# Kernel optimization log

Measured on AMD Instinct MI355X. Metric: run time of the kernel, lower is better.

The kernel has to match this reference:

```python
import jax, jax.numpy as jnp
import numpy as np

NUM_BUOYS = 16384
TIME_STEPS = 8
FEATURE_DIM = 64
ID_EMB_DIM = 1024  # must equal gru_hidden_size for steps 4/5 to type-check
HIDDEN = 1024
NUM_EMB = 100
INPUT_SIZE = FEATURE_DIM + ID_EMB_DIM


def setup_inputs() -> dict:
    key = jax.random.key(0)
    k = jax.random.split(key, 7)
    s = 1.0 / np.sqrt(HIDDEN)
    return {
        "buoy_obs": jax.random.normal(k[0], (NUM_BUOYS, TIME_STEPS, FEATURE_DIM), jnp.float32),
        "buoy_ids": jax.random.randint(k[1], (NUM_BUOYS,), 0, NUM_EMB),
        "emb": jax.random.normal(k[2], (NUM_EMB, ID_EMB_DIM), jnp.float32),
        "W_ih": jax.random.uniform(k[3], (3 * HIDDEN, INPUT_SIZE), jnp.float32, -s, s),
        "W_hh": jax.random.uniform(k[4], (3 * HIDDEN, HIDDEN), jnp.float32, -s, s),
        "b_ih": jax.random.uniform(k[5], (3 * HIDDEN,), jnp.float32, -s, s),
        "b_hh": jax.random.uniform(k[6], (3 * HIDDEN,), jnp.float32, -s, s),
    }


def _gru_cell(x, h, W_ih, W_hh, b_ih, b_hh):
    # PyTorch GRU gate layout: [r, z, n]
    gi = x @ W_ih.T + b_ih  # (N, 3H)
    gh = h @ W_hh.T + b_hh  # (N, 3H)
    gi_r, gi_z, gi_n = jnp.split(gi, 3, axis=-1)
    gh_r, gh_z, gh_n = jnp.split(gh, 3, axis=-1)
    r = jax.nn.sigmoid(gi_r + gh_r)
    z = jax.nn.sigmoid(gi_z + gh_z)
    n = jnp.tanh(gi_n + r * gh_n)
    return (1.0 - z) * n + z * h


def reference(buoy_obs, buoy_ids, emb, W_ih, W_hh, b_ih, b_hh):
    num_buoys = buoy_obs.shape[0]
    id_emb = emb[buoy_ids]  # (N, E)
    h = jnp.zeros((num_buoys, HIDDEN), buoy_obs.dtype)
    outs = []
    # three unrolled steps: input = [obs_t, id_emb]
    for t in range(3):
        x = jnp.concatenate([buoy_obs[:, t, :], id_emb], axis=-1)
        h = _gru_cell(x, h, W_ih, W_hh, b_ih, b_hh)
        outs.append(h)
    # step 4: input = [out0, obs_1]
    x = jnp.concatenate([outs[0], buoy_obs[:, 1, :]], axis=-1)
    h = _gru_cell(x, h, W_ih, W_hh, b_ih, b_hh)
    second_out = h
    # step 5: input = [out4, obs_2]
    x = jnp.concatenate([second_out, buoy_obs[:, 2, :]], axis=-1)
    h = _gru_cell(x, h, W_ih, W_hh, b_ih, b_hh)
    # AdaptiveMaxPool1d(1) over a length-1 time axis is identity
    return h[None, :, :]  # (1, N, H)
```

## Files before the change

kernel.cpp:

```cpp
#include <hip/hip_runtime.h>
#include <hip/hip_bf16.h>


typedef __bf16 bf16_4 __attribute__((ext_vector_type(4)));
typedef __bf16 bf16_8 __attribute__((ext_vector_type(8)));
typedef float  f32_16 __attribute__((ext_vector_type(16)));

#define NBUOY 16384
#define HID   1024

__device__ __forceinline__ void async16(const void* g, void* l) {
    __builtin_amdgcn_global_load_lds(
        (const __attribute__((address_space(1))) unsigned int*)g,
        (__attribute__((address_space(3))) unsigned int*)l, 16, 0, 0);
}
__device__ __forceinline__ float sigm(float x)  { return 1.f / (1.f + __expf(-x)); }
__device__ __forceinline__ float tanh_f(float x){ return 1.f - 2.f / (1.f + __expf(2.f * x)); }

template<int QN, int K>
__device__ __forceinline__ void phase_loop(
    const __bf16* __restrict__ Ap, long sA, int aRow0,
    const __bf16* __restrict__ Wp, long sW, int n0,
    __bf16* lsA, __bf16* lsB, f32_16 acc[4][2], int tid)
{
    const int lane = tid & 63, wid = tid >> 6;
    const int wm = wid >> 1, wn = wid & 1;
    const int l31 = lane & 31, hi = lane >> 5, l7 = lane & 7;
    const int srow = tid >> 3, schunk = tid & 7;

    #pragma unroll 1
    for (int k0 = 0; k0 < K; k0 += 64) {
        __syncthreads();
        #pragma unroll
        for (int r = 0; r < 4; ++r) {
            int row = r * 32 + srow;
            int lc  = schunk ^ (row & 7);
            async16(Ap + (long)(aRow0 + row) * sA + k0 + lc * 8,
                    lsA + (r * 32 + wid * 8) * 64);
        }
        #pragma unroll
        for (int r = 0; r < 6; ++r) {
            int brow = r * 32 + srow;
            int lc   = schunk ^ (brow & 7);
            async16(Wp + (long)((brow >> 6) * 1024 + n0 + (brow & 63)) * sW + k0 + lc * 8,
                    lsB + (r * 32 + wid * 8) * 64);
        }
        __syncthreads();
        #pragma unroll
        for (int ks = 0; ks < 4; ++ks) {
            int pc = (((ks * 2 + hi) ^ l7)) * 8;
            bf16_8 a0 = *(const bf16_8*)(lsA + (wm * 64 +      l31) * 64 + pc);
            bf16_8 a1 = *(const bf16_8*)(lsA + (wm * 64 + 32 + l31) * 64 + pc);
            bf16_8 br = *(const bf16_8*)(lsB + (        wn * 32 + l31) * 64 + pc);
            bf16_8 bz = *(const bf16_8*)(lsB + ( 64 +   wn * 32 + l31) * 64 + pc);
            bf16_8 bn = *(const bf16_8*)(lsB + (128 +   wn * 32 + l31) * 64 + pc);
            acc[0][0]  = __builtin_amdgcn_mfma_f32_32x32x16_bf16(a0, br, acc[0][0], 0, 0, 0);
            acc[0][1]  = __builtin_amdgcn_mfma_f32_32x32x16_bf16(a1, br, acc[0][1], 0, 0, 0);
            acc[1][0]  = __builtin_amdgcn_mfma_f32_32x32x16_bf16(a0, bz, acc[1][0], 0, 0, 0);
            acc[1][1]  = __builtin_amdgcn_mfma_f32_32x32x16_bf16(a1, bz, acc[1][1], 0, 0, 0);
            acc[QN][0] = __builtin_amdgcn_mfma_f32_32x32x16_bf16(a0, bn, acc[QN][0], 0, 0, 0);
            acc[QN][1] = __builtin_amdgcn_mfma_f32_32x32x16_bf16(a1, bn, acc[QN][1], 0, 0, 0);
        }
    }
}

template<int KIH, int KHH, bool USE_E, bool OUT_F32>
__global__ __launch_bounds__(256, 2)
void gru_step(const __bf16* __restrict__ Aih, long sAih,
              const __bf16* __restrict__ Wih,
              const __bf16* __restrict__ Ahh,
              const __bf16* __restrict__ Whh,
              const float*  __restrict__ E,
              const int*    __restrict__ ids,
              const float*  __restrict__ bih,
              const float*  __restrict__ bhh,
              const __bf16* __restrict__ hprev,
              void* __restrict__ outp, long sOut)
{
    __shared__ __bf16 lsA[128 * 64];
    __shared__ __bf16 lsB[192 * 64];
    const int tid  = threadIdx.x;
    const int lane = tid & 63, wid = tid >> 6;
    const int wm = wid >> 1, wn = wid & 1;
    const int l31 = lane & 31, hi = lane >> 5;
    const int m0 = blockIdx.y * 128;
    const int n0 = blockIdx.x * 64;

    f32_16 acc[4][2];
    #pragma unroll
    for (int q = 0; q < 4; ++q)
        #pragma unroll
        for (int mt = 0; mt < 2; ++mt) acc[q][mt] = (f32_16)(0.0f);

    phase_loop<2, KIH>(Aih, sAih, m0, Wih, 1088, n0, lsA, lsB, acc, tid);
    if (KHH > 0)
        phase_loop<3, KHH>(Ahh, 1088, m0, Whh, 1024, n0, lsA, lsB, acc, tid);

    const int col = n0 + wn * 32 + l31;
    const float bhr = bhh[col], bhz = bhh[1024 + col], bhn = bhh[2048 + col];
    float cir = 0.f, ciz = 0.f, cin = 0.f;
    if (!USE_E) { cir = bih[col]; ciz = bih[1024 + col]; cin = bih[2048 + col]; }

    #pragma unroll
    for (int mt = 0; mt < 2; ++mt) {
        const int rowb = m0 + wm * 64 + mt * 32 + 4 * hi;
        #pragma unroll
        for (int reg = 0; reg < 16; ++reg) {
            const int row = rowb + (reg & 3) + 8 * (reg >> 2);
            float er = cir, ez = ciz, en = cin;
            if (USE_E) {
                const float* Ep = E + (long)ids[row] * 3072 + col;
                er = Ep[0]; ez = Ep[1024]; en = Ep[2048];
            }
            const float r  = sigm(acc[0][mt][reg] + er + bhr);
            const float z  = sigm(acc[1][mt][reg] + ez + bhz);
            const float nn = tanh_f(acc[2][mt][reg] + en + r * (acc[3][mt][reg] + bhn));
            float hp = 0.f;
            if (KHH > 0) hp = (float)hprev[(long)row * 1088 + col];
            const float h = (1.f - z) * nn + z * hp;
            if (OUT_F32) ((float*)outp)[(long)row * sOut + col] = h;
            else        ((__bf16*)outp)[(long)row * sOut + col] = (__bf16)h;
        }
    }
}

#define ETILE 10
__global__ void compute_E(const float* __restrict__ emb, const float* __restrict__ Wih,
                          const float* __restrict__ bih, float* __restrict__ E)
{
    __shared__ float semb[ETILE * 1024];
    const int e0 = blockIdx.x * ETILE;
    const int j  = blockIdx.y * 256 + threadIdx.x;
    for (int i = threadIdx.x; i < ETILE * 1024; i += 256)
        semb[i] = emb[(long)(e0 + (i >> 10)) * 1024 + (i & 1023)];
    __syncthreads();
    const float* wp = Wih + (long)j * 1088 + 64;
    float a[ETILE];
    const float b = bih[j];
    #pragma unroll
    for (int t = 0; t < ETILE; ++t) a[t] = b;
    for (int k = 0; k < 1024; k += 4) {
        const float4 w = *(const float4*)(wp + k);
        #pragma unroll
        for (int t = 0; t < ETILE; ++t) {
            const float* se = semb + t * 1024 + k;
            a[t] += se[0] * w.x + se[1] * w.y + se[2] * w.z + se[3] * w.w;
        }
    }
    #pragma unroll
    for (int t = 0; t < ETILE; ++t) E[(long)(e0 + t) * 3072 + j] = a[t];
}

__global__ void build_obs(const float* __restrict__ obs, __bf16* __restrict__ OBS,
                          __bf16* __restrict__ X0, __bf16* __restrict__ X1)
{
    const int q = blockIdx.x * 256 + threadIdx.x;
    const int row = q / 48, w = (q % 48) * 4;
    const float4 v = *(const float4*)(obs + (long)row * 512 + w);
    bf16_4 b; b[0] = (__bf16)v.x; b[1] = (__bf16)v.y; b[2] = (__bf16)v.z; b[3] = (__bf16)v.w;
    *(bf16_4*)(OBS + (long)row * 192 + w) = b;
    if (w >= 64 && w < 128) *(bf16_4*)(X0 + (long)row * 1088 + 1024 + (w - 64))  = b;
    if (w >= 128)           *(bf16_4*)(X1 + (long)row * 1088 + 1024 + (w - 128)) = b;
}

__global__ void cast_f32_bf16(const float* __restrict__ s, __bf16* __restrict__ d, int n4)
{
    const int i = blockIdx.x * 256 + threadIdx.x;
    if (i < n4) {
        const float4 v = ((const float4*)s)[i];
        bf16_4 b; b[0] = (__bf16)v.x; b[1] = (__bf16)v.y; b[2] = (__bf16)v.z; b[3] = (__bf16)v.w;
        ((bf16_4*)d)[i] = b;
    }
}

extern "C" void kernel_launch(void* const* d_in, const int* in_sizes, int n_in,
                              void* d_out, int out_size, void* d_ws, size_t ws_size,
                              hipStream_t stream)
{
    const float* obs = (const float*)d_in[0];
    const int*   ids = (const int*)  d_in[1];
    const float* emb = (const float*)d_in[2];
    const float* Wih = (const float*)d_in[3];
    const float* Whh = (const float*)d_in[4];
    const float* bih = (const float*)d_in[5];
    const float* bhh = (const float*)d_in[6];
    float* out = (float*)d_out;

    const size_t MB = 1 << 20;
    const size_t XB = (size_t)NBUOY * 1088 * 2;
    const size_t NEEDED = 21 * MB + 3 * XB;
    if (ws_size < NEEDED) return;

    char* ws = (char*)d_ws;
    float*  E   = (float*) ws;
    __bf16* Wb  = (__bf16*)(ws + 2 * MB);
    __bf16* Ub  = (__bf16*)(ws + 9 * MB);
    __bf16* OBS = (__bf16*)(ws + 15 * MB);
    __bf16* X0  = (__bf16*)(ws + 21 * MB);
    __bf16* X1  = (__bf16*)(ws + 21 * MB + XB);
    __bf16* X2  = (__bf16*)(ws + 21 * MB + 2 * XB);

    dim3 blk(256);
    dim3 gridG(HID / 64, NBUOY / 128);

    cast_f32_bf16<<<(3072 * 1088 / 4 + 255) / 256, blk, 0, stream>>>(Wih, Wb, 3072 * 1088 / 4);
    cast_f32_bf16<<<(3072 * 1024 / 4 + 255) / 256, blk, 0, stream>>>(Whh, Ub, 3072 * 1024 / 4);
    build_obs<<<NBUOY * 48 / 256, blk, 0, stream>>>(obs, OBS, X0, X1);
    compute_E<<<dim3(10, 12), blk, 0, stream>>>(emb, Wih, bih, E);

    gru_step<64, 0, true, false><<<gridG, blk, 0, stream>>>(
        OBS + 0, 192, Wb, nullptr, Ub, E, ids, bih, bhh, nullptr, X0, 1088);
    gru_step<64, 1024, true, false><<<gridG, blk, 0, stream>>>(
        OBS + 64, 192, Wb, X0, Ub, E, ids, bih, bhh, X0, X1, 1088);
    gru_step<64, 1024, true, false><<<gridG, blk, 0, stream>>>(
        OBS + 128, 192, Wb, X1, Ub, E, ids, bih, bhh, X1, X2, 1088);
    gru_step<1088, 1024, false, false><<<gridG, blk, 0, stream>>>(
        X0, 1088, Wb, X2, Ub, nullptr, ids, bih, bhh, X2, X1, 1088);
    gru_step<1088, 1024, false, true><<<gridG, blk, 0, stream>>>(
        X1, 1088, Wb, X1, Ub, nullptr, ids, bih, bhh, X1, out, 1024);
}
```

Baseline: 983.9 us.

## Warp-specialize GRU GEMM into producer/consumer waves with triple-buffered LDS ring

Splits each 512-thread block into four producer waves that issue async global-to-LDS loads into a 3-stage ring buffer and four consumer waves that run the MFMA loop. The stages are coordinated with shared-memory ready/done counters and spin-waits instead of block barriers. The aim is to overlap memory loads with matrix math and drop the per-k-step double __syncthreads. In exchange it uses much more LDS per block, which may cut occupancy, and adds spin-wait overhead plus a flattened 1D grid.

```diff
diff --git a/kernel.cpp b/kernel.cpp
--- a/kernel.cpp
+++ b/kernel.cpp
@@ -17,55 +17,30 @@
 __device__ __forceinline__ float sigm(float x)  { return 1.f / (1.f + __expf(-x)); }
 __device__ __forceinline__ float tanh_f(float x){ return 1.f - 2.f / (1.f + __expf(2.f * x)); }
 
-template<int QN, int K>
-__device__ __forceinline__ void phase_loop(
-    const __bf16* __restrict__ Ap, long sA, int aRow0,
-    const __bf16* __restrict__ Wp, long sW, int n0,
-    __bf16* lsA, __bf16* lsB, f32_16 acc[4][2], int tid)
-{
-    const int lane = tid & 63, wid = tid >> 6;
-    const int wm = wid >> 1, wn = wid & 1;
-    const int l31 = lane & 31, hi = lane >> 5, l7 = lane & 7;
-    const int srow = tid >> 3, schunk = tid & 7;
-
-    #pragma unroll 1
-    for (int k0 = 0; k0 < K; k0 += 64) {
-        __syncthreads();
-        #pragma unroll
-        for (int r = 0; r < 4; ++r) {
-            int row = r * 32 + srow;
-            int lc  = schunk ^ (row & 7);
-            async16(Ap + (long)(aRow0 + row) * sA + k0 + lc * 8,
-                    lsA + (r * 32 + wid * 8) * 64);
-        }
-        #pragma unroll
-        for (int r = 0; r < 6; ++r) {
-            int brow = r * 32 + srow;
-            int lc   = schunk ^ (brow & 7);
-            async16(Wp + (long)((brow >> 6) * 1024 + n0 + (brow & 63)) * sW + k0 + lc * 8,
-                    lsB + (r * 32 + wid * 8) * 64);
-        }
-        __syncthreads();
-        #pragma unroll
-        for (int ks = 0; ks < 4; ++ks) {
-            int pc = (((ks * 2 + hi) ^ l7)) * 8;
-            bf16_8 a0 = *(const bf16_8*)(lsA + (wm * 64 +      l31) * 64 + pc);
-            bf16_8 a1 = *(const bf16_8*)(lsA + (wm * 64 + 32 + l31) * 64 + pc);
-            bf16_8 br = *(const bf16_8*)(lsB + (        wn * 32 + l31) * 64 + pc);
-            bf16_8 bz = *(const bf16_8*)(lsB + ( 64 +   wn * 32 + l31) * 64 + pc);
-            bf16_8 bn = *(const bf16_8*)(lsB + (128 +   wn * 32 + l31) * 64 + pc);
-            acc[0][0]  = __builtin_amdgcn_mfma_f32_32x32x16_bf16(a0, br, acc[0][0], 0, 0, 0);
-            acc[0][1]  = __builtin_amdgcn_mfma_f32_32x32x16_bf16(a1, br, acc[0][1], 0, 0, 0);
-            acc[1][0]  = __builtin_amdgcn_mfma_f32_32x32x16_bf16(a0, bz, acc[1][0], 0, 0, 0);
-            acc[1][1]  = __builtin_amdgcn_mfma_f32_32x32x16_bf16(a1, bz, acc[1][1], 0, 0, 0);
-            acc[QN][0] = __builtin_amdgcn_mfma_f32_32x32x16_bf16(a0, bn, acc[QN][0], 0, 0, 0);
-            acc[QN][1] = __builtin_amdgcn_mfma_f32_32x32x16_bf16(a1, bn, acc[QN][1], 0, 0, 0);
-        }
+template<int QN>
+__device__ __forceinline__ void cons_iter(const __bf16* lsA, const __bf16* lsB,
+                                          f32_16 acc[4][2], int wm, int wn, int l31, int hi)
+{
+    const int l7 = l31 & 7;
+    #pragma unroll
+    for (int ks = 0; ks < 4; ++ks) {
+        const int pc = ((2 * ks + hi) ^ l7) * 8;
+        bf16_8 a0 = *(const bf16_8*)(lsA + (wm * 64 +      l31) * 64 + pc);
+        bf16_8 a1 = *(const bf16_8*)(lsA + (wm * 64 + 32 + l31) * 64 + pc);
+        bf16_8 br = *(const bf16_8*)(lsB + (       wn * 32 + l31) * 64 + pc);
+        bf16_8 bz = *(const bf16_8*)(lsB + ( 64 +  wn * 32 + l31) * 64 + pc);
+        bf16_8 bn = *(const bf16_8*)(lsB + (128 +  wn * 32 + l31) * 64 + pc);
+        acc[0][0]  = __builtin_amdgcn_mfma_f32_32x32x16_bf16(a0, br, acc[0][0], 0, 0, 0);
+        acc[0][1]  = __builtin_amdgcn_mfma_f32_32x32x16_bf16(a1, br, acc[0][1], 0, 0, 0);
+        acc[1][0]  = __builtin_amdgcn_mfma_f32_32x32x16_bf16(a0, bz, acc[1][0], 0, 0, 0);
+        acc[1][1]  = __builtin_amdgcn_mfma_f32_32x32x16_bf16(a1, bz, acc[1][1], 0, 0, 0);
+        acc[QN][0] = __builtin_amdgcn_mfma_f32_32x32x16_bf16(a0, bn, acc[QN][0], 0, 0, 0);
+        acc[QN][1] = __builtin_amdgcn_mfma_f32_32x32x16_bf16(a1, bn, acc[QN][1], 0, 0, 0);
     }
 }
 
 template<int KIH, int KHH, bool USE_E, bool OUT_F32>
-__global__ __launch_bounds__(256, 2)
+__global__ __launch_bounds__(512, 2)
 void gru_step(const __bf16* __restrict__ Aih, long sAih,
               const __bf16* __restrict__ Wih,
               const __bf16* __restrict__ Ahh,
@@ -77,14 +52,60 @@
               const __bf16* __restrict__ hprev,
               void* __restrict__ outp, long sOut)
 {
-    __shared__ __bf16 lsA[128 * 64];
-    __shared__ __bf16 lsB[192 * 64];
-    const int tid  = threadIdx.x;
-    const int lane = tid & 63, wid = tid >> 6;
+    constexpr int T1 = KIH / 64, T2 = KHH / 64, T = T1 + T2;
+    __shared__ __bf16 stage[3][320 * 64];
+    __shared__ int ready[3];
+    __shared__ int done[3];
+
+    const int tid = threadIdx.x;
+    if (tid < 3) { ready[tid] = 0; done[tid] = 0; }
+    __syncthreads();
+
+    const int wid = tid >> 6, lane = tid & 63;
+    const int bid = blockIdx.x;
+    const int n0  = (bid & 15) * 64;
+    const int m0  = (bid >> 4) * 128;
+
+    if (wid >= 4) {
+        const int pw = wid - 4;
+        const int ptid = tid - 256;
+        const int srow = ptid >> 3, sch = ptid & 7;
+        #pragma unroll 1
+        for (int i = 0; i < T; ++i) {
+            const int s = i % 3;
+            if (i >= 3) {
+                const int tgt = 4 * (i / 3);
+                while (((volatile int*)done)[s] < tgt) __builtin_amdgcn_s_sleep(1);
+                asm volatile("" ::: "memory");
+            }
+            const __bf16* Ap; long sA; const __bf16* Wp; long sW; int k0;
+            if (i < T1) { Ap = Aih; sA = sAih; Wp = Wih; sW = 1088; k0 = i * 64; }
+            else        { Ap = Ahh; sA = 1088; Wp = Whh; sW = 1024; k0 = (i - T1) * 64; }
+            __bf16* lsA = &stage[s][0];
+            __bf16* lsB = &stage[s][128 * 64];
+            #pragma unroll
+            for (int r = 0; r < 4; ++r) {
+                int row = r * 32 + srow;
+                int lc  = sch ^ (row & 7);
+                async16(Ap + (long)(m0 + row) * sA + k0 + lc * 8,
+                        lsA + (r * 32 + pw * 8) * 64);
+            }
+            #pragma unroll
+            for (int r = 0; r < 6; ++r) {
+                int brow = r * 32 + srow;
+                int lc   = sch ^ (brow & 7);
+                async16(Wp + (long)((brow >> 6) * 1024 + n0 + (brow & 63)) * sW + k0 + lc * 8,
+                        lsB + (r * 32 + pw * 8) * 64);
+            }
+            asm volatile("s_waitcnt vmcnt(0)" ::: "memory");
+            __threadfence_block();
+            if (lane == 0) atomicAdd(&ready[s], 1);
+        }
+        return;
+    }
+
     const int wm = wid >> 1, wn = wid & 1;
     const int l31 = lane & 31, hi = lane >> 5;
-    const int m0 = blockIdx.y * 128;
-    const int n0 = blockIdx.x * 64;
 
     f32_16 acc[4][2];
     #pragma unroll
@@ -92,9 +113,19 @@
         #pragma unroll
         for (int mt = 0; mt < 2; ++mt) acc[q][mt] = (f32_16)(0.0f);
 
-    phase_loop<2, KIH>(Aih, sAih, m0, Wih, 1088, n0, lsA, lsB, acc, tid);
-    if (KHH > 0)
-        phase_loop<3, KHH>(Ahh, 1088, m0, Whh, 1024, n0, lsA, lsB, acc, tid);
+    #pragma unroll 1
+    for (int i = 0; i < T; ++i) {
+        const int s = i % 3;
+        const int tgt = 4 * (i / 3 + 1);
+        while (((volatile int*)ready)[s] < tgt) __builtin_amdgcn_s_sleep(1);
+        asm volatile("" ::: "memory");
+        const __bf16* lsA = &stage[s][0];
+        const __bf16* lsB = &stage[s][128 * 64];
+        if (i < T1) cons_iter<2>(lsA, lsB, acc, wm, wn, l31, hi);
+        else        cons_iter<3>(lsA, lsB, acc, wm, wn, l31, hi);
+        asm volatile("" ::: "memory");
+        if (lane == 0) atomicAdd(&done[s], 1);
+    }
 
     const int col = n0 + wn * 32 + l31;
     const float bhr = bhh[col], bhz = bhh[1024 + col], bhn = bhh[2048 + col];
@@ -201,21 +232,22 @@
     __bf16* X2  = (__bf16*)(ws + 21 * MB + 2 * XB);
 
     dim3 blk(256);
-    dim3 gridG(HID / 64, NBUOY / 128);
+    dim3 blkG(512);
+    dim3 gridG(2048);
 
     cast_f32_bf16<<<(3072 * 1088 / 4 + 255) / 256, blk, 0, stream>>>(Wih, Wb, 3072 * 1088 / 4);
     cast_f32_bf16<<<(3072 * 1024 / 4 + 255) / 256, blk, 0, stream>>>(Whh, Ub, 3072 * 1024 / 4);
     build_obs<<<NBUOY * 48 / 256, blk, 0, stream>>>(obs, OBS, X0, X1);
     compute_E<<<dim3(10, 12), blk, 0, stream>>>(emb, Wih, bih, E);
 
-    gru_step<64, 0, true, false><<<gridG, blk, 0, stream>>>(
+    gru_step<64, 0, true, false><<<gridG, blkG, 0, stream>>>(
         OBS + 0, 192, Wb, nullptr, Ub, E, ids, bih, bhh, nullptr, X0, 1088);
-    gru_step<64, 1024, true, false><<<gridG, blk, 0, stream>>>(
+    gru_step<64, 1024, true, false><<<gridG, blkG, 0, stream>>>(
         OBS + 64, 192, Wb, X0, Ub, E, ids, bih, bhh, X0, X1, 1088);
-    gru_step<64, 1024, true, false><<<gridG, blk, 0, stream>>>(
+    gru_step<64, 1024, true, false><<<gridG, blkG, 0, stream>>>(
         OBS + 128, 192, Wb, X1, Ub, E, ids, bih, bhh, X1, X2, 1088);
-    gru_step<1088, 1024, false, false><<<gridG, blk, 0, stream>>>(
+    gru_step<1088, 1024, false, false><<<gridG, blkG, 0, stream>>>(
         X0, 1088, Wb, X2, Ub, nullptr, ids, bih, bhh, X2, X1, 1088);
-    gru_step<1088, 1024, false, true><<<gridG, blk, 0, stream>>>(
+    gru_step<1088, 1024, false, true><<<gridG, blkG, 0, stream>>>(
         X1, 1088, Wb, X1, Ub, nullptr, ids, bih, bhh, X1, out, 1024);
 }
```

Result: slower. 3.373 ms (+242.8%).
